# Kernel tuning notes

Measured on AMD Instinct MI355X. Metric: run time of the kernel, lower is better.

The kernel has to match this reference:

```python
import jax, jax.numpy as jnp
import numpy as np

N_NODES = 100000
N_HEDGES = 100000
N_INC = 1000000
IN_DIM = 128
SEL_THRESHOLD = 0.5  # aug_node assumption: select nodes with low overlappness
EPS = 1e-10


def setup_inputs() -> dict:
    key = jax.random.key(0)
    ks = jax.random.split(key, 8)
    X = jax.random.normal(ks[0], (N_NODES, IN_DIM), dtype=jnp.float32)
    W1 = jax.random.normal(ks[1], (IN_DIM, IN_DIM // 2), dtype=jnp.float32) * 0.1
    b1 = jnp.zeros((IN_DIM // 2,), jnp.float32)
    W2 = jax.random.normal(ks[2], (IN_DIM // 2, 3), dtype=jnp.float32) * 0.1
    b2 = jnp.zeros((3,), jnp.float32)
    overlappness = jax.random.uniform(ks[3], (N_NODES,), dtype=jnp.float32)
    gumbel_u = jax.random.uniform(ks[4], (N_HEDGES, 3), dtype=jnp.float32)
    nodes = jax.random.randint(ks[5], (N_INC,), 0, N_NODES, dtype=jnp.int32)
    hedges = jax.random.randint(ks[6], (N_INC,), 0, N_HEDGES, dtype=jnp.int32)
    edge_index = jnp.stack([nodes, hedges], axis=0)
    return {"X": X, "W1": W1, "b1": b1, "W2": W2, "b2": b2,
            "overlappness": overlappness, "gumbel_u": gumbel_u,
            "edge_index": edge_index}


def _hypergraph_conv(X, ei0, ei1, W, b, n_nodes, n_hedges):
    # out = D^-1 H B^-1 H^T (X @ W) + b  (PyG HypergraphConv, unit edge weights)
    Xt = X @ W
    ones = jnp.ones((ei0.shape[0],), Xt.dtype)
    B = jax.ops.segment_sum(ones, ei1, num_segments=n_hedges)   # hyperedge degree
    D = jax.ops.segment_sum(ones, ei0, num_segments=n_nodes)    # node degree
    Binv = jnp.where(B > 0, 1.0 / B, 0.0)
    Dinv = jnp.where(D > 0, 1.0 / D, 0.0)
    Xe = jax.ops.segment_sum(Xt[ei0], ei1, num_segments=n_hedges) * Binv[:, None]
    Xn = jax.ops.segment_sum(Xe[ei1], ei0, num_segments=n_nodes) * Dinv[:, None]
    return Xn + b


def reference(X, W1, b1, W2, b2, overlappness, gumbel_u, edge_index):
    ei0 = edge_index[0]
    ei1 = edge_index[1]
    n_nodes = X.shape[0]
    n_hedges = gumbel_u.shape[0]

    # two-layer hypergraph encoder
    H1 = _hypergraph_conv(X, ei0, ei1, W1, b1, n_nodes, n_hedges)
    H2 = _hypergraph_conv(H1, ei0, ei1, W2, b2, n_nodes, n_hedges)  # [N, 3]

    # per-hyperedge scatter-mean of gathered node features
    ones = jnp.ones((ei0.shape[0],), H2.dtype)
    cnt = jax.ops.segment_sum(ones, ei1, num_segments=n_hedges)
    Xe = jax.ops.segment_sum(H2[ei0], ei1, num_segments=n_hedges)
    Xe = Xe * jnp.where(cnt > 0, 1.0 / cnt, 0.0)[:, None]

    # sigmoid + row-sum normalize (scale is detached in the original)
    Xe = jax.nn.sigmoid(Xe)
    rowsum = jax.lax.stop_gradient(jnp.sum(Xe, axis=1, keepdims=True))
    Xe = Xe * jnp.where(rowsum != 0, 1.0 / rowsum, 0.0)

    # gumbel-softmax (tau=1, hard) with explicit uniform noise
    g = -jnp.log(-jnp.log(gumbel_u + EPS) + EPS)
    y_soft = jax.nn.softmax(Xe + g, axis=-1)
    hard = jax.nn.one_hot(jnp.argmax(y_soft, axis=-1), 3, dtype=y_soft.dtype)

    sel_mask = (overlappness < SEL_THRESHOLD).astype(H2.dtype)  # aug_node
    reserve_f = hard[:, 0][ei1]                       # reserve edges
    mask_f = hard[:, 2][ei1] * sel_mask[ei0]          # masked-but-selected
    sample = jnp.maximum(reserve_f, mask_f)           # logical OR on {0,1}

    # jit-safe stand-in for edge_index[:, sample]: dropped columns -> -1
    keep = sample > 0
    edge_index_out = jnp.where(keep[None, :], edge_index, -1)
    return sample.astype(jnp.float32), edge_index_out
```

## Files before the change

### kernel.cpp

```cpp
#include <hip/hip_runtime.h>
#include <math.h>

#define N_NODES   100000
#define N_HEDGES  100000
#define N_INC     1000000
#define IN_DIM    128
#define SHIFT     7
#define BMASK     127
#define NBKT      782
#define CAP       2048
#define NBLK      245
#define BT        1024

typedef unsigned int u32;

__global__ void __launch_bounds__(256)
init_kernel(const float* __restrict__ W1, const float* __restrict__ b1,
            const float* __restrict__ W2, float* __restrict__ W12,
            float* __restrict__ cvec, int* __restrict__ gcur) {
    int blk = blockIdx.x, t = threadIdx.x;
    if (blk == 0) {
        if (t < 128) {
            float a0 = 0.f, a1 = 0.f, a2 = 0.f;
            for (int m = 0; m < 64; ++m) {
                float ww = W1[t * 64 + m];
                a0 += ww * W2[m * 3 + 0];
                a1 += ww * W2[m * 3 + 1];
                a2 += ww * W2[m * 3 + 2];
            }
            W12[t * 3 + 0] = a0; W12[t * 3 + 1] = a1; W12[t * 3 + 2] = a2;
        }
        if (t < 3) {
            float c = 0.f;
            for (int m = 0; m < 64; ++m) c += b1[m] * W2[m * 3 + t];
            cvec[t] = c;
        }
    } else {
        int i = (blk - 1) * 256 + t;
        if (i < 25024) gcur[i] = 0;
    }
}

__global__ void __launch_bounds__(BT)
build_kernel(const int* __restrict__ ei0, const int* __restrict__ ei1,
             int* __restrict__ gcur, u32* __restrict__ payload_n,
             u32* __restrict__ payload_h)
{
    __shared__ int hA[NBKT], hB[NBKT];
    int blk = blockIdx.x, t = threadIdx.x;

    for (int i = t; i < NBKT; i += BT) { hA[i] = 0; hB[i] = 0; }
    __syncthreads();
    int i4 = blk * BT + t;
    bool ok = (i4 * 4 < N_INC);
    int4 n4 = ok ? ((const int4*)ei0)[i4] : make_int4(0, 0, 0, 0);
    int4 h4 = ok ? ((const int4*)ei1)[i4] : make_int4(0, 0, 0, 0);
    int nn[4] = {n4.x, n4.y, n4.z, n4.w};
    int hv[4] = {h4.x, h4.y, h4.z, h4.w};
    int rn[4], rh[4];
    if (ok) {
        #pragma unroll
        for (int e = 0; e < 4; ++e) {
            rn[e] = atomicAdd(&hA[nn[e] >> SHIFT], 1);
            rh[e] = atomicAdd(&hB[hv[e] >> SHIFT], 1);
        }
    }
    __syncthreads();
    for (int i = t; i < NBKT; i += BT) {
        int c = hA[i];
        if (c) hA[i] = i * CAP + atomicAdd(&gcur[i * 16], c);
        c = hB[i];
        if (c) hB[i] = i * CAP + atomicAdd(&gcur[(NBKT + i) * 16], c);
    }
    __syncthreads();
    if (ok) {
        #pragma unroll
        for (int e = 0; e < 4; ++e) {
            int n = nn[e], h = hv[e];
            payload_n[hA[n >> SHIFT] + rn[e]] = ((u32)(n & BMASK) << 17) | (u32)h;
            payload_h[hB[h >> SHIFT] + rh[e]] = ((u32)(h & BMASK) << 17) | (u32)n;
        }
    }
}

__global__ void __launch_bounds__(256)
gemm_z_kernel(const float* __restrict__ X, const float* __restrict__ W12,
              float* __restrict__ Z, int n_nodes) {
    int t = threadIdx.x;
    int grp = t >> 5, l = t & 31;
    float w0[4], w1[4], w2[4];
    #pragma unroll
    for (int i = 0; i < 4; ++i) {
        int k = 4 * l + i;
        w0[i] = W12[k * 3 + 0];
        w1[i] = W12[k * 3 + 1];
        w2[i] = W12[k * 3 + 2];
    }
    int node = blockIdx.x * 8 + grp;
    if (node >= n_nodes) return;
    float4 x4 = ((const float4*)(X + (size_t)node * IN_DIM))[l];
    float a0 = x4.x * w0[0] + x4.y * w0[1] + x4.z * w0[2] + x4.w * w0[3];
    float a1 = x4.x * w1[0] + x4.y * w1[1] + x4.z * w1[2] + x4.w * w1[3];
    float a2 = x4.x * w2[0] + x4.y * w2[1] + x4.z * w2[2] + x4.w * w2[3];
    #pragma unroll
    for (int off = 16; off > 0; off >>= 1) {
        a0 += __shfl_xor(a0, off);
        a1 += __shfl_xor(a1, off);
        a2 += __shfl_xor(a2, off);
    }
    if (l == 0) {
        Z[(size_t)node * 4 + 0] = a0;
        Z[(size_t)node * 4 + 1] = a1;
        Z[(size_t)node * 4 + 2] = a2;
        Z[(size_t)node * 4 + 3] = 0.f;
    }
}

__global__ void __launch_bounds__(256)
phase2_kernel(const u32* __restrict__ payload_n, const u32* __restrict__ payload_h,
              const int* __restrict__ gcur,
              u32* __restrict__ od_n, u32* __restrict__ od_h,
              int* __restrict__ slot_n, int* __restrict__ slot_h)
{
    __shared__ int hist[128], curs[128];
    int t = threadIdx.x;
    int bk = blockIdx.x;
    int dir = (bk >= NBKT) ? 1 : 0;
    int b = bk - dir * NBKT;
    const u32* payload = dir ? payload_h : payload_n;
    u32* od   = dir ? od_h   : od_n;
    int* slot = dir ? slot_h : slot_n;
    int tot = gcur[bk * 16];
    int base = b * CAP;

    if (t < 128) hist[t] = 0;
    __syncthreads();
    for (int j = t; j < tot; j += 256) atomicAdd(&hist[payload[base + j] >> 17], 1);
    __syncthreads();
    if (t < 64) {
        int lane = t;
        int h0 = hist[lane], h1 = hist[64 + lane];
        int s0 = h0, s1 = h1;
        #pragma unroll
        for (int d = 1; d < 64; d <<= 1) {
            int u0 = __shfl_up(s0, d), u1 = __shfl_up(s1, d);
            if (lane >= d) { s0 += u0; s1 += u1; }
        }
        int tot0 = __shfl(s0, 63);
        int e0 = s0 - h0, e1 = tot0 + s1 - h1;
        int d0 = (b << SHIFT) + lane, d1 = d0 + 64;
        if (d0 < N_NODES) od[d0] = ((u32)(base + e0) << 10) | (u32)h0;
        if (d1 < N_NODES) od[d1] = ((u32)(base + e1) << 10) | (u32)h1;
        curs[lane] = e0; curs[64 + lane] = e1;
    }
    __syncthreads();
    for (int j = t; j < tot; j += 256) {
        u32 p = payload[base + j];
        int r = atomicAdd(&curs[p >> 17], 1);
        slot[base + r] = (int)(p & 0x1FFFF);
    }
}

__global__ void gather_kernel(const float* __restrict__ src, float* __restrict__ dst,
                              const u32* __restrict__ od, const int* __restrict__ slot,
                              const float* __restrict__ addv, int nrows) {
    int tid = blockIdx.x * blockDim.x + threadIdx.x;
    int r = tid >> 3, sub = tid & 7;
    if (r >= nrows) return;
    u32 v = od[r];
    int s = (int)(v >> 10), deg = (int)(v & 1023);
    float a0 = 0.f, a1 = 0.f, a2 = 0.f;
    for (int j = s + sub; j < s + deg; j += 8) {
        float4 x = ((const float4*)src)[slot[j]];
        a0 += x.x; a1 += x.y; a2 += x.z;
    }
    a0 += __shfl_xor(a0, 1); a1 += __shfl_xor(a1, 1); a2 += __shfl_xor(a2, 1);
    a0 += __shfl_xor(a0, 2); a1 += __shfl_xor(a1, 2); a2 += __shfl_xor(a2, 2);
    a0 += __shfl_xor(a0, 4); a1 += __shfl_xor(a1, 4); a2 += __shfl_xor(a2, 4);
    if (sub == 0) {
        float inv = deg > 0 ? 1.0f / (float)deg : 0.f;
        float b0 = 0.f, b1 = 0.f, b2 = 0.f;
        if (addv) { b0 = addv[0]; b1 = addv[1]; b2 = addv[2]; }
        ((float4*)dst)[r] = make_float4(a0 * inv + b0, a1 * inv + b1, a2 * inv + b2, 0.f);
    }
}

__global__ void hedge_final_kernel(const float* __restrict__ H2,
                                   const u32* __restrict__ od_h, const int* __restrict__ slot_h,
                                   const float* __restrict__ gu, float* __restrict__ hard0,
                                   float* __restrict__ hard2, int n) {
    int tid = blockIdx.x * blockDim.x + threadIdx.x;
    int h = tid >> 3, sub = tid & 7;
    if (h >= n) return;
    u32 v = od_h[h];
    int s = (int)(v >> 10), deg = (int)(v & 1023);
    float a0 = 0.f, a1 = 0.f, a2 = 0.f;
    for (int j = s + sub; j < s + deg; j += 8) {
        float4 x = ((const float4*)H2)[slot_h[j]];
        a0 += x.x; a1 += x.y; a2 += x.z;
    }
    a0 += __shfl_xor(a0, 1); a1 += __shfl_xor(a1, 1); a2 += __shfl_xor(a2, 1);
    a0 += __shfl_xor(a0, 2); a1 += __shfl_xor(a1, 2); a2 += __shfl_xor(a2, 2);
    a0 += __shfl_xor(a0, 4); a1 += __shfl_xor(a1, 4); a2 += __shfl_xor(a2, 4);
    if (sub != 0) return;
    float binv = deg > 0 ? 1.0f / (float)deg : 0.f;
    float s0 = a0 * binv, s1 = a1 * binv, s2 = a2 * binv;
    float x0 = 1.0f / (1.0f + expf(-s0));
    float x1 = 1.0f / (1.0f + expf(-s1));
    float x2 = 1.0f / (1.0f + expf(-s2));
    float rs = x0 + x1 + x2;
    float rinv = rs != 0.f ? 1.0f / rs : 0.f;
    x0 *= rinv; x1 *= rinv; x2 *= rinv;
    const float EPS = 1e-10f;
    float g0 = -logf(-logf(gu[(size_t)h * 3 + 0] + EPS) + EPS);
    float g1 = -logf(-logf(gu[(size_t)h * 3 + 1] + EPS) + EPS);
    float g2 = -logf(-logf(gu[(size_t)h * 3 + 2] + EPS) + EPS);
    float v0 = x0 + g0, v1 = x1 + g1, v2 = x2 + g2;
    int am = 0; float vm = v0;
    if (v1 > vm) { am = 1; vm = v1; }
    if (v2 > vm) { am = 2; vm = v2; }
    hard0[h] = (am == 0) ? 1.f : 0.f;
    hard2[h] = (am == 2) ? 1.f : 0.f;
}

__global__ void edge_final_kernel(const float* __restrict__ hard0, const float* __restrict__ hard2,
                                  const float* __restrict__ ov,
                                  const int* __restrict__ ei0, const int* __restrict__ ei1,
                                  float* __restrict__ out, int n4) {
    int i4 = blockIdx.x * blockDim.x + threadIdx.x;
    if (i4 >= n4) return;
    int4 n4v = ((const int4*)ei0)[i4];
    int4 h4v = ((const int4*)ei1)[i4];
    int nn[4] = {n4v.x, n4v.y, n4v.z, n4v.w};
    int hh[4] = {h4v.x, h4v.y, h4v.z, h4v.w};
    float smp[4], oi[4], oh[4];
    #pragma unroll
    for (int e = 0; e < 4; ++e) {
        float r = hard0[hh[e]];
        float m = hard2[hh[e]] * (ov[nn[e]] < 0.5f ? 1.f : 0.f);
        float s = fmaxf(r, m);
        smp[e] = s;
        bool keep = s > 0.f;
        oi[e] = keep ? (float)nn[e] : -1.f;
        oh[e] = keep ? (float)hh[e] : -1.f;
    }
    ((float4*)out)[i4] = make_float4(smp[0], smp[1], smp[2], smp[3]);
    ((float4*)(out + N_INC))[i4] = make_float4(oi[0], oi[1], oi[2], oi[3]);
    ((float4*)(out + 2 * (size_t)N_INC))[i4] = make_float4(oh[0], oh[1], oh[2], oh[3]);
}

extern "C" void kernel_launch(void* const* d_in, const int* in_sizes, int n_in,
                              void* d_out, int out_size, void* d_ws, size_t ws_size,
                              hipStream_t stream) {
    const float* X  = (const float*)d_in[0];
    const float* W1 = (const float*)d_in[1];
    const float* b1 = (const float*)d_in[2];
    const float* W2 = (const float*)d_in[3];
    const float* b2 = (const float*)d_in[4];
    const float* ov = (const float*)d_in[5];
    const float* gu = (const float*)d_in[6];
    const int*   ei = (const int*)d_in[7];
    const int* ei0 = ei;
    const int* ei1 = ei + N_INC;

    int* ip = (int*)d_ws;
    int* gcur      = ip;
    u32* payload_n = (u32*)(gcur + 25024);
    u32* payload_h = payload_n + NBKT * CAP;
    int* slot_n    = (int*)(payload_h + NBKT * CAP);
    int* slot_h    = slot_n + NBKT * CAP;
    u32* od_n      = (u32*)(slot_h + NBKT * CAP);
    u32* od_h      = od_n + 100096;
    float* W12     = (float*)(od_h + 100096);
    float* cvec    = W12 + 384;
    float* Z       = cvec + 16;
    float* XeA     = Z    + 4 * N_NODES;
    float* XnA     = XeA  + 4 * N_HEDGES;
    float* XeB     = XnA  + 4 * N_NODES;
    float* XnB     = XeB  + 4 * N_HEDGES;
    float* hard0   = XnB  + 4 * N_NODES;
    float* hard2   = hard0 + N_HEDGES;

    const int TB = 256;
    int gOct = (8 * N_NODES + TB - 1) / TB;

    init_kernel<<<99, 256, 0, stream>>>(W1, b1, W2, W12, cvec, gcur);
    build_kernel<<<NBLK, BT, 0, stream>>>(ei0, ei1, gcur, payload_n, payload_h);
    gemm_z_kernel<<<(N_NODES + 7) / 8, 256, 0, stream>>>(X, W12, Z, N_NODES);
    phase2_kernel<<<2 * NBKT, 256, 0, stream>>>(payload_n, payload_h, gcur,
                                                od_n, od_h, slot_n, slot_h);

    gather_kernel<<<gOct, TB, 0, stream>>>(Z,   XeA, od_h, slot_h, nullptr, N_HEDGES);
    gather_kernel<<<gOct, TB, 0, stream>>>(XeA, XnA, od_n, slot_n, cvec,    N_NODES);
    gather_kernel<<<gOct, TB, 0, stream>>>(XnA, XeB, od_h, slot_h, nullptr, N_HEDGES);
    gather_kernel<<<gOct, TB, 0, stream>>>(XeB, XnB, od_n, slot_n, b2,      N_NODES);

    hedge_final_kernel<<<gOct, TB, 0, stream>>>(XnB, od_h, slot_h, gu, hard0, hard2, N_HEDGES);

    edge_final_kernel<<<(N_INC / 4 + TB - 1) / TB, TB, 0, stream>>>(hard0, hard2, ov, ei0, ei1,
                                                                    (float*)d_out, N_INC / 4);
}
```

Before: 126.7 us.

## Fuse CSR build with Z GEMM and first gather into phase2

Runs the X·W12 projection in extra blocks of the bucket-build kernel, so the bandwidth-heavy GEMM overlaps with the atomic-heavy bucketing. The first hyperedge gather is appended to the hyperedge-direction blocks of phase2, which removes one kernel launch and reads the just-written slot list while it is likely still cached. That gather now uses only 2 threads per hyperedge instead of 8, which may lengthen it, and it relies on Z being complete before phase2 starts.

```diff
diff --git a/kernel.cpp b/kernel.cpp
--- a/kernel.cpp
+++ b/kernel.cpp
@@ -10,6 +10,8 @@
 #define NBKT      782
 #define CAP       2048
 #define NBLK      245
+#define GEMM_BLKS 267
+#define NGRP      (GEMM_BLKS * 32)
 #define BT        1024
 
 typedef unsigned int u32;
@@ -42,85 +44,87 @@
 }
 
 __global__ void __launch_bounds__(BT)
-build_kernel(const int* __restrict__ ei0, const int* __restrict__ ei1,
-             int* __restrict__ gcur, u32* __restrict__ payload_n,
-             u32* __restrict__ payload_h)
+fused_bg_kernel(const int* __restrict__ ei0, const int* __restrict__ ei1,
+                const float* __restrict__ X, const float* __restrict__ W12,
+                int* __restrict__ gcur, u32* __restrict__ payload_n,
+                u32* __restrict__ payload_h, float* __restrict__ Z)
 {
     __shared__ int hA[NBKT], hB[NBKT];
     int blk = blockIdx.x, t = threadIdx.x;
 
-    for (int i = t; i < NBKT; i += BT) { hA[i] = 0; hB[i] = 0; }
-    __syncthreads();
-    int i4 = blk * BT + t;
-    bool ok = (i4 * 4 < N_INC);
-    int4 n4 = ok ? ((const int4*)ei0)[i4] : make_int4(0, 0, 0, 0);
-    int4 h4 = ok ? ((const int4*)ei1)[i4] : make_int4(0, 0, 0, 0);
-    int nn[4] = {n4.x, n4.y, n4.z, n4.w};
-    int hv[4] = {h4.x, h4.y, h4.z, h4.w};
-    int rn[4], rh[4];
-    if (ok) {
+    if (blk < NBLK) {
+        for (int i = t; i < NBKT; i += BT) { hA[i] = 0; hB[i] = 0; }
+        __syncthreads();
+        int i4 = blk * BT + t;
+        bool ok = (i4 * 4 < N_INC);
+        int4 n4 = ok ? ((const int4*)ei0)[i4] : make_int4(0, 0, 0, 0);
+        int4 h4 = ok ? ((const int4*)ei1)[i4] : make_int4(0, 0, 0, 0);
+        int nn[4] = {n4.x, n4.y, n4.z, n4.w};
+        int hv[4] = {h4.x, h4.y, h4.z, h4.w};
+        int rn[4], rh[4];
+        if (ok) {
+            #pragma unroll
+            for (int e = 0; e < 4; ++e) {
+                rn[e] = atomicAdd(&hA[nn[e] >> SHIFT], 1);
+                rh[e] = atomicAdd(&hB[hv[e] >> SHIFT], 1);
+            }
+        }
+        __syncthreads();
+        for (int i = t; i < NBKT; i += BT) {
+            int c = hA[i];
+            if (c) hA[i] = i * CAP + atomicAdd(&gcur[i * 16], c);
+            c = hB[i];
+            if (c) hB[i] = i * CAP + atomicAdd(&gcur[(NBKT + i) * 16], c);
+        }
+        __syncthreads();
+        if (ok) {
+            #pragma unroll
+            for (int e = 0; e < 4; ++e) {
+                int n = nn[e], h = hv[e];
+                payload_n[hA[n >> SHIFT] + rn[e]] = ((u32)(n & BMASK) << 17) | (u32)h;
+                payload_h[hB[h >> SHIFT] + rh[e]] = ((u32)(h & BMASK) << 17) | (u32)n;
+            }
+        }
+    } else {
+        float* wl = (float*)hA;
+        if (t < 384) wl[t] = W12[t];
+        __syncthreads();
+        int grp = t >> 5, l = t & 31;
+        float w0[4], w1[4], w2[4];
         #pragma unroll
-        for (int e = 0; e < 4; ++e) {
-            rn[e] = atomicAdd(&hA[nn[e] >> SHIFT], 1);
-            rh[e] = atomicAdd(&hB[hv[e] >> SHIFT], 1);
-        }
-    }
-    __syncthreads();
-    for (int i = t; i < NBKT; i += BT) {
-        int c = hA[i];
-        if (c) hA[i] = i * CAP + atomicAdd(&gcur[i * 16], c);
-        c = hB[i];
-        if (c) hB[i] = i * CAP + atomicAdd(&gcur[(NBKT + i) * 16], c);
-    }
-    __syncthreads();
-    if (ok) {
-        #pragma unroll
-        for (int e = 0; e < 4; ++e) {
-            int n = nn[e], h = hv[e];
-            payload_n[hA[n >> SHIFT] + rn[e]] = ((u32)(n & BMASK) << 17) | (u32)h;
-            payload_h[hB[h >> SHIFT] + rh[e]] = ((u32)(h & BMASK) << 17) | (u32)n;
+        for (int i = 0; i < 4; ++i) {
+            int k = 4 * l + i;
+            w0[i] = wl[k * 3 + 0];
+            w1[i] = wl[k * 3 + 1];
+            w2[i] = wl[k * 3 + 2];
+        }
+        for (int node = (blk - NBLK) * 32 + grp; node < N_NODES; node += NGRP) {
+            float4 x4 = ((const float4*)(X + (size_t)node * IN_DIM))[l];
+            float a0 = x4.x * w0[0] + x4.y * w0[1] + x4.z * w0[2] + x4.w * w0[3];
+            float a1 = x4.x * w1[0] + x4.y * w1[1] + x4.z * w1[2] + x4.w * w1[3];
+            float a2 = x4.x * w2[0] + x4.y * w2[1] + x4.z * w2[2] + x4.w * w2[3];
+            #pragma unroll
+            for (int off = 16; off > 0; off >>= 1) {
+                a0 += __shfl_xor(a0, off);
+                a1 += __shfl_xor(a1, off);
+                a2 += __shfl_xor(a2, off);
+            }
+            if (l == 0) {
+                Z[(size_t)node * 4 + 0] = a0;
+                Z[(size_t)node * 4 + 1] = a1;
+                Z[(size_t)node * 4 + 2] = a2;
+                Z[(size_t)node * 4 + 3] = 0.f;
+            }
         }
     }
 }
 
 __global__ void __launch_bounds__(256)
-gemm_z_kernel(const float* __restrict__ X, const float* __restrict__ W12,
-              float* __restrict__ Z, int n_nodes) {
-    int t = threadIdx.x;
-    int grp = t >> 5, l = t & 31;
-    float w0[4], w1[4], w2[4];
-    #pragma unroll
-    for (int i = 0; i < 4; ++i) {
-        int k = 4 * l + i;
-        w0[i] = W12[k * 3 + 0];
-        w1[i] = W12[k * 3 + 1];
-        w2[i] = W12[k * 3 + 2];
-    }
-    int node = blockIdx.x * 8 + grp;
-    if (node >= n_nodes) return;
-    float4 x4 = ((const float4*)(X + (size_t)node * IN_DIM))[l];
-    float a0 = x4.x * w0[0] + x4.y * w0[1] + x4.z * w0[2] + x4.w * w0[3];
-    float a1 = x4.x * w1[0] + x4.y * w1[1] + x4.z * w1[2] + x4.w * w1[3];
-    float a2 = x4.x * w2[0] + x4.y * w2[1] + x4.z * w2[2] + x4.w * w2[3];
-    #pragma unroll
-    for (int off = 16; off > 0; off >>= 1) {
-        a0 += __shfl_xor(a0, off);
-        a1 += __shfl_xor(a1, off);
-        a2 += __shfl_xor(a2, off);
-    }
-    if (l == 0) {
-        Z[(size_t)node * 4 + 0] = a0;
-        Z[(size_t)node * 4 + 1] = a1;
-        Z[(size_t)node * 4 + 2] = a2;
-        Z[(size_t)node * 4 + 3] = 0.f;
-    }
-}
-
-__global__ void __launch_bounds__(256)
-phase2_kernel(const u32* __restrict__ payload_n, const u32* __restrict__ payload_h,
-              const int* __restrict__ gcur,
-              u32* __restrict__ od_n, u32* __restrict__ od_h,
-              int* __restrict__ slot_n, int* __restrict__ slot_h)
+phase2_g1_kernel(const u32* __restrict__ payload_n, const u32* __restrict__ payload_h,
+                 const int* __restrict__ gcur, const float* __restrict__ Z,
+                 u32* __restrict__ od_n, u32* __restrict__ od_h,
+                 int* __restrict__ slot_n, int* __restrict__ slot_h,
+                 float* __restrict__ XeA)
 {
     __shared__ int hist[128], curs[128];
     int t = threadIdx.x;
@@ -158,6 +162,24 @@
         u32 p = payload[base + j];
         int r = atomicAdd(&curs[p >> 17], 1);
         slot[base + r] = (int)(p & 0x1FFFF);
+    }
+    if (!dir) return;
+
+    __syncthreads();
+    int row = t >> 1, sub = t & 1;
+    int h = (b << SHIFT) + row;
+    if (h >= N_HEDGES) return;
+    u32 v = od_h[h];
+    int s = (int)(v >> 10), deg = (int)(v & 1023);
+    float a0 = 0.f, a1 = 0.f, a2 = 0.f;
+    for (int j = s + sub; j < s + deg; j += 2) {
+        float4 x = ((const float4*)Z)[slot_h[j]];
+        a0 += x.x; a1 += x.y; a2 += x.z;
+    }
+    a0 += __shfl_xor(a0, 1); a1 += __shfl_xor(a1, 1); a2 += __shfl_xor(a2, 1);
+    if (sub == 0) {
+        float inv = deg > 0 ? 1.0f / (float)deg : 0.f;
+        ((float4*)XeA)[h] = make_float4(a0 * inv, a1 * inv, a2 * inv, 0.f);
     }
 }
 
@@ -285,13 +307,12 @@
     int gOct = (8 * N_NODES + TB - 1) / TB;
 
     init_kernel<<<99, 256, 0, stream>>>(W1, b1, W2, W12, cvec, gcur);
-    build_kernel<<<NBLK, BT, 0, stream>>>(ei0, ei1, gcur, payload_n, payload_h);
-    gemm_z_kernel<<<(N_NODES + 7) / 8, 256, 0, stream>>>(X, W12, Z, N_NODES);
-    phase2_kernel<<<2 * NBKT, 256, 0, stream>>>(payload_n, payload_h, gcur,
-                                                od_n, od_h, slot_n, slot_h);
-
-    gather_kernel<<<gOct, TB, 0, stream>>>(Z,   XeA, od_h, slot_h, nullptr, N_HEDGES);
-    gather_kernel<<<gOct, TB, 0, stream>>>(XeA, XnA, od_n, slot_n, cvec,    N_NODES);
+    fused_bg_kernel<<<NBLK + GEMM_BLKS, BT, 0, stream>>>(ei0, ei1, X, W12, gcur,
+                                                         payload_n, payload_h, Z);
+    phase2_g1_kernel<<<2 * NBKT, 256, 0, stream>>>(payload_n, payload_h, gcur, Z,
+                                                   od_n, od_h, slot_n, slot_h, XeA);
+
+    gather_kernel<<<gOct, TB, 0, stream>>>(XeA, XnA, od_n, slot_n, cvec, N_NODES);
     gather_kernel<<<gOct, TB, 0, stream>>>(XnA, XeB, od_h, slot_h, nullptr, N_HEDGES);
     gather_kernel<<<gOct, TB, 0, stream>>>(XeB, XnB, od_n, slot_n, b2,      N_NODES);
 
```

Result: no change. 125.9 us (-0.6%).
